# Optimization experiments

Measured on AMD Instinct MI355X. Metric: run time of the kernel, lower is better.

Reference implementation:

```python
import math
import jax, jax.numpy as jnp
import numpy as np

N, E, D, B, S, H = 16384, 196608, 256, 256, 64, 8
DH = D // H
BN_INV = 1.0 / math.sqrt(1.0 + 1e-5)  # eval-mode BN: mean=0, var=1, eps=1e-5
LOG2 = math.log(2.0)


def _mlp(x, w1, b1, w2, b2):
    # Linear -> SiLU -> Linear
    return jax.nn.silu(x @ w1 + b1) @ w2 + b2


def _bn(x, g, b):
    # BatchNorm1d in eval mode with running_mean=0, running_var=1
    return x * (BN_INV * g) + b


def _graph_ln(x, g, b):
    # pyg LayerNorm(mode='graph') called with batch=None: normalize over all nodes+features
    mu = jnp.mean(x)
    xc = x - mu
    var = jnp.mean(xc * xc)
    return xc * jax.lax.rsqrt(var + 1e-5) * g + b


def _forward(x, edge_index, edge_attr,
             node_w1, node_b1, node_w2, node_b2,
             c_w1, c_b1, c_w2, c_b2,
             bn_e_g, bn_e_b, bn_h_g, bn_h_b,
             n1l_g, n1l_b, n1a_g, n1a_b, n2_g, n2_b,
             wq, bq, wk, bk, wv, bv, wo, bo,
             aff_w1, aff_b1, aff_w2, aff_b2,
             fn_g, fn_b, fc_w1, fc_b1, fc_w2, fc_b2):
    row, col = edge_index[0], edge_index[1]

    # ---- PotNetConvGate local branch ----
    # A, B, V, U MLPs (all take node features) computed with stacked weights [4,D,D]
    hid = jax.nn.silu(jnp.einsum('nd,kdf->knf', x, node_w1) + node_b1[:, None, :])
    node_out = jnp.einsum('knf,kfg->kng', hid, node_w2) + node_b2[:, None, :]
    h_A, h_B, h_V, h_U = node_out[0], node_out[1], node_out[2], node_out[3]
    e_C = _mlp(edge_attr, c_w1, c_b1, c_w2, c_b2)  # [E,D]

    score = jax.nn.relu(_bn(h_A[row] + h_B[col] + e_C, bn_e_g, bn_e_b))  # [E,D]
    e_new = edge_attr + score

    # pyg softmax over edges grouped by destination node (col), per channel
    m = jax.ops.segment_max(e_new, col, num_segments=N)        # [N,D]
    ex = jnp.exp(e_new - m[col])
    s = jax.ops.segment_sum(ex, col, num_segments=N)           # [N,D]
    gated = ex / (s[col] + 1e-16)

    msg = gated * (h_V[col] + e_new)
    aggr = jax.ops.segment_sum(msg, col, num_segments=N)       # [N,D]
    h_local = jax.nn.silu(x + _bn(h_U + aggr, bn_h_g, bn_h_b))
    # e_out = silu(e_new + edge_attr)  # edge output, not used downstream for node output
    h_local = _bn(h_local, n1l_g, n1l_b)  # norm1_local

    # ---- global Transformer branch (equal-size graphs -> dense reshape, full mask) ----
    hd = x.reshape(B, S, D)
    q = (hd @ wq + bq).reshape(B, S, H, DH).transpose(0, 2, 1, 3)
    k = (hd @ wk + bk).reshape(B, S, H, DH).transpose(0, 2, 1, 3)
    v = (hd @ wv + bv).reshape(B, S, H, DH).transpose(0, 2, 1, 3)
    att = jax.nn.softmax(jnp.einsum('bhqd,bhkd->bhqk', q, k) / math.sqrt(DH), axis=-1)
    o = jnp.einsum('bhqk,bhkd->bhqd', att, v).transpose(0, 2, 1, 3).reshape(B, S, D)
    h_attn = (o @ wo + bo).reshape(N, D)

    h_attn = _bn(h_attn + x, n1a_g, n1a_b)  # norm1_attn
    t = jax.nn.gelu(h_attn @ aff_w1 + aff_b1, approximate=False) @ aff_w2 + aff_b2
    h_attn = _graph_ln(t + x, fn_g, fn_b)   # feed_norm

    # ---- fuse branches (mean over stacked outputs) ----
    h_new = (h_local + h_attn) * 0.5

    # ---- _ff_block: fc = Linear -> ShiftedSoftplus -> Linear ----
    ssp = jax.nn.softplus(h_new @ fc_w1 + fc_b1) - LOG2
    out = ssp @ fc_w2 + fc_b2
    return _bn(out + h_new, n2_g, n2_b)  # norm2


def setup_inputs():
    key = jax.random.key(0)
    ks = iter(jax.random.split(key, 64))
    sc = 1.0 / math.sqrt(D)
    def w(shape):
        return jax.random.normal(next(ks), shape, jnp.float32) * sc
    z = lambda *s: jnp.zeros(s, jnp.float32)
    o = lambda *s: jnp.ones(s, jnp.float32)
    return {
        'x': jax.random.normal(next(ks), (N, D), jnp.float32),
        'edge_index': jax.random.randint(next(ks), (2, E), 0, N, jnp.int32),
        'edge_attr': jax.random.normal(next(ks), (E, D), jnp.float32),
        'node_w1': w((4, D, D)), 'node_b1': z(4, D),
        'node_w2': w((4, D, D)), 'node_b2': z(4, D),
        'c_w1': w((D, D)), 'c_b1': z(D), 'c_w2': w((D, D)), 'c_b2': z(D),
        'bn_e_g': o(D), 'bn_e_b': z(D), 'bn_h_g': o(D), 'bn_h_b': z(D),
        'n1l_g': o(D), 'n1l_b': z(D), 'n1a_g': o(D), 'n1a_b': z(D),
        'n2_g': o(D), 'n2_b': z(D),
        'wq': w((D, D)), 'bq': z(D), 'wk': w((D, D)), 'bk': z(D),
        'wv': w((D, D)), 'bv': z(D), 'wo': w((D, D)), 'bo': z(D),
        'aff_w1': w((D, 2 * D)), 'aff_b1': z(2 * D),
        'aff_w2': w((2 * D, D)), 'aff_b2': z(D),
        'fn_g': o(D), 'fn_b': z(D),
        'fc_w1': w((D, 2 * D)), 'fc_b1': z(2 * D),
        'fc_w2': w((2 * D, D)), 'fc_b2': z(D),
    }


def reference(x, edge_index, edge_attr,
              node_w1, node_b1, node_w2, node_b2,
              c_w1, c_b1, c_w2, c_b2,
              bn_e_g, bn_e_b, bn_h_g, bn_h_b,
              n1l_g, n1l_b, n1a_g, n1a_b, n2_g, n2_b,
              wq, bq, wk, bk, wv, bv, wo, bo,
              aff_w1, aff_b1, aff_w2, aff_b2,
              fn_g, fn_b, fc_w1, fc_b1, fc_w2, fc_b2):
    return _forward(x, edge_index, edge_attr,
                    node_w1, node_b1, node_w2, node_b2,
                    c_w1, c_b1, c_w2, c_b2,
                    bn_e_g, bn_e_b, bn_h_g, bn_h_b,
                    n1l_g, n1l_b, n1a_g, n1a_b, n2_g, n2_b,
                    wq, bq, wk, bk, wv, bv, wo, bo,
                    aff_w1, aff_b1, aff_w2, aff_b2,
                    fn_g, fn_b, fc_w1, fc_b1, fc_w2, fc_b2)
```

## Files before the change

### kernel.cpp

```cpp
#include <hip/hip_runtime.h>
#include <hip/hip_bf16.h>
#include <stdint.h>

#define NN 16384
#define NE 196608
#define DD 256
#define ND 4194304
#define BNINV 0.9999950000374997f
#define LOG2F_ 0.6931471805599453f

typedef __attribute__((ext_vector_type(8))) short short8v;
typedef __attribute__((ext_vector_type(4))) float float4v;

__device__ __forceinline__ float b2f(__hip_bfloat16 v) { return __bfloat162float(v); }
__device__ __forceinline__ __hip_bfloat16 f2b(float v) { return __float2bfloat16(v); }

__device__ __forceinline__ void gl_lds16(const __hip_bfloat16* g, __hip_bfloat16* l) {
  __builtin_amdgcn_global_load_lds((const __attribute__((address_space(1))) void*)g,
                                   (__attribute__((address_space(3))) void*)l, 16, 0, 0);
}

__device__ __forceinline__ float rdf(const void* p, size_t i, int fl) {
  return fl ? b2f(((const __hip_bfloat16*)p)[i]) : ((const float*)p)[i];
}

#define OFF_WT    0ul
#define OFF_PB    2883584ul
#define OFF_XB    2899968ul
#define OFF_HN    11288576ul
#define OFF_HL    44843008ul
#define OFF_HIDE  61620224ul
#define OFF_EN    162283520ul
#define OFF_QKV   262946816ul
#define OFF_O     313278464ul
#define OFF_HATTN 321667072ul
#define OFF_HIDN  330055680ul
#define OFF_U     346832896ul
#define OFF_HNEW  363610112ul
#define OFF_HNEWB 380387328ul
#define OFF_TAIL  388775936ul

#define PB_NB1   0
#define PB_NB2   1024
#define PB_CB1   2048
#define PB_CB2   2304
#define PB_QKVB  2560
#define PB_BO    3328
#define PB_AB1   3584
#define PB_AB2   4096
#define PB_FB1   4352
#define PB_FB2   4864
#define PB_BNEG  5120
#define PB_BNEB  5376
#define PB_BNHG  5632
#define PB_BNHB  5888
#define PB_N1LG  6144
#define PB_N1LB  6400
#define PB_N1AG  6656
#define PB_N1AB  6912
#define PB_N2G   7168
#define PB_N2B   7424
#define PB_FNG   7680
#define PB_FNB   7936

__global__ void probe_kernel(const uint32_t* bneg_raw, int* flag) {
  if (threadIdx.x == 0 && blockIdx.x == 0)
    *flag = (bneg_raw[0] == 0x3F803F80u) ? 1 : 0;
}

struct PJobs {
  const void* src[24];
  int off[24];
  int len[24];
};

__global__ void canon_params(PJobs jb, __hip_bfloat16* PB, const int* flagp) {
  const int fl = *flagp;
  const int j = blockIdx.x;
  const void* src = jb.src[j];
  const int off = jb.off[j], len = jb.len[j];
  for (int i = threadIdx.x; i < len; i += 256) PB[off + i] = f2b(rdf(src, i, fl));
}

__global__ void canon_x(const void* x, __hip_bfloat16* XB, const int* flagp) {
  const int fl = *flagp;
  const size_t i = (size_t)blockIdx.x * 256 + threadIdx.x;
  XB[i] = f2b(rdf(x, i, fl));
}

struct TJobsF {
  const void* src[18];
  __hip_bfloat16* dst[18];
  int R[18];
  int C[18];
  int RB[18];
};

__global__ void transpose_rb(TJobsF jb, const int* flagp) {
  __shared__ __hip_bfloat16 tile[32][33];
  const int fl = *flagp;
  const int j = blockIdx.z;
  const int R = jb.R[j], C = jb.C[j], RB = jb.RB[j];
  const int c0 = blockIdx.x * 32, r0 = blockIdx.y * 32;
  if (c0 >= C || r0 >= R) return;
  const void* src = jb.src[j];
  __hip_bfloat16* dst = jb.dst[j];
  const int tx = threadIdx.x, ty = threadIdx.y;
#pragma unroll
  for (int i = 0; i < 4; ++i)
    tile[ty + i * 8][tx] = f2b(rdf(src, (size_t)(RB + r0 + ty + i * 8) * C + c0 + tx, fl));
  __syncthreads();
#pragma unroll
  for (int i = 0; i < 4; ++i)
    dst[(long)(c0 + ty + i * 8) * R + r0 + tx] = tile[tx][ty + i * 8];
}

__global__ void prep_kernel(int* counts, double* stats) {
  const int i = blockIdx.x * blockDim.x + threadIdx.x;
  if (i < NN) counts[i] = 0;
  if (i == 0) counts[NN] = 0;
  if (i < 2) stats[i] = 0.0;
}

template <int ACT, int RES, int BNM, int OUTBF, int ASRC, int DUALOUT>
__global__ __launch_bounds__(256) void gemm_bt(
    const void* __restrict__ Avp, const __hip_bfloat16* __restrict__ Wt,
    const __hip_bfloat16* __restrict__ bias, const void* __restrict__ Res,
    const __hip_bfloat16* __restrict__ bng, const __hip_bfloat16* __restrict__ bnb,
    void* __restrict__ Cout, const int* __restrict__ flagp,
    int M, int N, int K, long boff, long az, long wz, long bz, long cz) {
  __shared__ __align__(16) __hip_bfloat16 sA[128 * 32];
  __shared__ __align__(16) __hip_bfloat16 sB[128 * 32];
  const int fl = (ASRC || DUALOUT) ? *flagp : 1;
  const int z = blockIdx.z;
  const long aoff = boff + (long)z * az;
  const __hip_bfloat16* Ab = (const __hip_bfloat16*)Avp + aoff;
  const float* Af = (const float*)Avp + aoff;
  Wt += (long)z * wz;
  bias += (long)z * bz;
  const long coff = (long)z * cz;
  const int tid = threadIdx.x;
  const int lane = tid & 63;
  const int wid = tid >> 6;
  const int wm = wid >> 1, wn = wid & 1;
  const int l16 = lane & 15, lq = lane >> 4;
  const long am0 = (long)blockIdx.y * 128;
  const long bn0 = (long)blockIdx.x * 128;

  float4v acc[4][4] = {};

  const int nK = K >> 5;
  for (int kb = 0; kb < nK; ++kb) {
    if (ASRC == 1 && fl == 0) {
#pragma unroll
      for (int r = 0; r < 2; ++r) {
        const int c = tid + r * 256;
        const float* ap = Af + (am0 + (c >> 2)) * K + kb * 32 + (c & 3) * 8;
        const float4v f0 = *(const float4v*)ap;
        const float4v f1 = *(const float4v*)(ap + 4);
        short8v s;
#pragma unroll
        for (int i = 0; i < 4; ++i) {
          __hip_bfloat16 h0 = f2b(f0[i]), h1 = f2b(f1[i]);
          s[i] = *(short*)&h0;
          s[4 + i] = *(short*)&h1;
        }
        ((short8v*)sA)[c] = s;
        gl_lds16(Wt + (bn0 + (c >> 2)) * K + kb * 32 + (c & 3) * 8, sB + c * 8);
      }
    } else {
#pragma unroll
      for (int r = 0; r < 2; ++r) {
        const int c = tid + r * 256;
        gl_lds16(Ab + (am0 + (c >> 2)) * K + kb * 32 + (c & 3) * 8, sA + c * 8);
        gl_lds16(Wt + (bn0 + (c >> 2)) * K + kb * 32 + (c & 3) * 8, sB + c * 8);
      }
    }
    __syncthreads();
    const short* pA = (const short*)sA;
    const short* pB = (const short*)sB;
    short8v af[4], bv_[4];
#pragma unroll
    for (int mi = 0; mi < 4; ++mi)
      af[mi] = *(const short8v*)(pA + (wm * 64 + mi * 16 + l16) * 32 + lq * 8);
#pragma unroll
    for (int ni = 0; ni < 4; ++ni)
      bv_[ni] = *(const short8v*)(pB + (wn * 64 + ni * 16 + l16) * 32 + lq * 8);
#pragma unroll
    for (int mi = 0; mi < 4; ++mi)
#pragma unroll
      for (int ni = 0; ni < 4; ++ni)
        acc[mi][ni] =
            __builtin_amdgcn_mfma_f32_16x16x32_bf16(af[mi], bv_[ni], acc[mi][ni], 0, 0, 0);
    __syncthreads();
  }

  const __hip_bfloat16* Rb = (const __hip_bfloat16*)Res;
  const float* Rf = (const float*)Res;
#pragma unroll
  for (int mi = 0; mi < 4; ++mi) {
#pragma unroll
    for (int ni = 0; ni < 4; ++ni) {
#pragma unroll
      for (int r = 0; r < 4; ++r) {
        const long row = am0 + wm * 64 + mi * 16 + lq * 4 + r;
        const long col = bn0 + wn * 64 + ni * 16 + l16;
        float v = acc[mi][ni][r] + b2f(bias[col]);
        if (ACT == 1) v = v / (1.f + __expf(-v));
        else if (ACT == 2) v = 0.5f * v * (1.f + erff(v * 0.7071067811865476f));
        else if (ACT == 3) v = (v > 15.f ? v : log1pf(__expf(v))) - LOG2F_;
        if (RES == 1) v += b2f(Rb[row * N + col]);
        else if (RES == 2) v += Rf[row * N + col];
        if (BNM) v = v * (BNINV * b2f(bng[col])) + b2f(bnb[col]);
        if (DUALOUT) {
          if (fl) ((__hip_bfloat16*)Cout)[coff + row * N + col] = f2b(v);
          else ((float*)Cout)[coff + row * N + col] = v;
        } else if (OUTBF) {
          ((__hip_bfloat16*)Cout)[coff + row * N + col] = f2b(v);
        } else {
          ((float*)Cout)[coff + row * N + col] = v;
        }
      }
    }
  }
}

__global__ __launch_bounds__(256) void gemm_edge2(
    const __hip_bfloat16* __restrict__ A, const __hip_bfloat16* __restrict__ Wt,
    const __hip_bfloat16* __restrict__ bias, const int* __restrict__ ei,
    const void* __restrict__ eattr, const __hip_bfloat16* __restrict__ HA,
    __hip_bfloat16* __restrict__ EN, const __hip_bfloat16* __restrict__ PB,
    const int* __restrict__ perm, const int* __restrict__ flagp) {
  __shared__ __align__(16) __hip_bfloat16 sA[128 * 32];
  __shared__ __align__(16) __hip_bfloat16 sB[128 * 32];
  const int fl = *flagp;
  const int tid = threadIdx.x;
  const int lane = tid & 63;
  const int wid = tid >> 6;
  const int wm = wid >> 1, wn = wid & 1;
  const int l16 = lane & 15, lq = lane >> 4;
  const long am0 = (long)blockIdx.y * 128;
  const long bn0 = (long)blockIdx.x * 128;
  const __hip_bfloat16* HB = HA + (size_t)ND;

  float4v acc[4][4] = {};

  const int K = DD;
  for (int kb = 0; kb < (K >> 5); ++kb) {
#pragma unroll
    for (int r = 0; r < 2; ++r) {
      const int c = tid + r * 256;
      gl_lds16(A + (am0 + (c >> 2)) * K + kb * 32 + (c & 3) * 8, sA + c * 8);
      gl_lds16(Wt + (bn0 + (c >> 2)) * K + kb * 32 + (c & 3) * 8, sB + c * 8);
    }
    __syncthreads();
    const short* pA = (const short*)sA;
    const short* pB = (const short*)sB;
    short8v af[4], bv_[4];
#pragma unroll
    for (int mi = 0; mi < 4; ++mi)
      af[mi] = *(const short8v*)(pA + (wm * 64 + mi * 16 + l16) * 32 + lq * 8);
#pragma unroll
    for (int ni = 0; ni < 4; ++ni)
      bv_[ni] = *(const short8v*)(pB + (wn * 64 + ni * 16 + l16) * 32 + lq * 8);
#pragma unroll
    for (int mi = 0; mi < 4; ++mi)
#pragma unroll
      for (int ni = 0; ni < 4; ++ni)
        acc[mi][ni] =
            __builtin_amdgcn_mfma_f32_16x16x32_bf16(af[mi], bv_[ni], acc[mi][ni], 0, 0, 0);
    __syncthreads();
  }

#pragma unroll
  for (int mi = 0; mi < 4; ++mi) {
#pragma unroll
    for (int r = 0; r < 4; ++r) {
      const long row = am0 + wm * 64 + mi * 16 + lq * 4 + r;
      const long ge = row;
      const int rr = ei[ge];
      const int cc = ei[NE + ge];
      const long pe = perm[ge];
#pragma unroll
      for (int ni = 0; ni < 4; ++ni) {
        const long col = bn0 + wn * 64 + ni * 16 + l16;
        float v = acc[mi][ni][r] + b2f(bias[col]);
        v += b2f(HA[(size_t)rr * DD + col]) + b2f(HB[(size_t)cc * DD + col]);
        v = v * (BNINV * b2f(PB[PB_BNEG + col])) + b2f(PB[PB_BNEB + col]);
        v = fmaxf(v, 0.f);
        v += rdf(eattr, (size_t)ge * DD + col, fl);
        EN[(size_t)pe * DD + col] = f2b(v);
      }
    }
  }
}

__global__ void count_kernel(const int* __restrict__ ei, int* __restrict__ counts) {
  const int e = blockIdx.x * 256 + threadIdx.x;
  if (e < NE) atomicAdd(&counts[ei[NE + e]], 1);
}

__global__ __launch_bounds__(1024) void scan_kernel(int* __restrict__ counts,
                                                    int* __restrict__ cursor) {
  __shared__ int part[1024];
  const int t = threadIdx.x;
  const int base = t * 16;
  int ss = 0;
#pragma unroll
  for (int i = 0; i < 16; ++i) ss += counts[base + i];
  part[t] = ss;
  __syncthreads();
  for (int off = 1; off < 1024; off <<= 1) {
    int v = (t >= off) ? part[t - off] : 0;
    __syncthreads();
    part[t] += v;
    __syncthreads();
  }
  int run = part[t] - ss;
  for (int i = 0; i < 16; ++i) {
    const int cv = counts[base + i];
    counts[base + i] = run;
    cursor[base + i] = run;
    run += cv;
  }
  if (t == 1023) counts[NN] = run;
}

__global__ void scatter_kernel(const int* __restrict__ ei, int* __restrict__ cursor,
                               int* __restrict__ perm) {
  const int e = blockIdx.x * 256 + threadIdx.x;
  if (e < NE) {
    const int p = atomicAdd(&cursor[ei[NE + e]], 1);
    perm[e] = p;
  }
}

__global__ __launch_bounds__(256) void segment_kernel(
    const int* __restrict__ offs, const __hip_bfloat16* __restrict__ EN,
    const __hip_bfloat16* __restrict__ hV, const __hip_bfloat16* __restrict__ hU,
    const __hip_bfloat16* __restrict__ XB, const __hip_bfloat16* __restrict__ PB,
    float* __restrict__ hlocal) {
  const int n = blockIdx.x;
  const int d = threadIdx.x;
  const int beg = offs[n], end = offs[n + 1];
  float sa = 0.f, sb = 0.f;
  int p = beg;
  for (; p + 4 <= end; p += 4) {
    const float v0 = b2f(EN[(size_t)(p + 0) * DD + d]);
    const float v1 = b2f(EN[(size_t)(p + 1) * DD + d]);
    const float v2 = b2f(EN[(size_t)(p + 2) * DD + d]);
    const float v3 = b2f(EN[(size_t)(p + 3) * DD + d]);
    const float e0 = __expf(v0), e1 = __expf(v1), e2 = __expf(v2), e3 = __expf(v3);
    sa += (e0 + e1) + (e2 + e3);
    sb += (e0 * v0 + e1 * v1) + (e2 * v2 + e3 * v3);
  }
  for (; p < end; ++p) {
    const float v = b2f(EN[(size_t)p * DD + d]);
    const float e = __expf(v);
    sa += e;
    sb += e * v;
  }
  const float hv = b2f(hV[(size_t)n * DD + d]);
  const float ag = (hv * sa + sb) / (sa + 1e-16f);
  const float t1 =
      (b2f(hU[(size_t)n * DD + d]) + ag) * (BNINV * b2f(PB[PB_BNHG + d])) + b2f(PB[PB_BNHB + d]);
  float s1 = b2f(XB[(size_t)n * DD + d]) + t1;
  s1 = s1 / (1.f + __expf(-s1));
  s1 = s1 * (BNINV * b2f(PB[PB_N1LG + d])) + b2f(PB[PB_N1LB + d]);
  hlocal[(size_t)n * DD + d] = s1;
}

__global__ __launch_bounds__(256) void attn_kernel(const float* __restrict__ QKV,
                                                   __hip_bfloat16* __restrict__ O) {
  __shared__ float sq[64][33], sk[64][33], sv[64][33];
  __shared__ float sp[64][65];
  const int bh = blockIdx.x;
  const int b = bh >> 3, h = bh & 7;
  const int tid = threadIdx.x;
  const float* Q = QKV;
  const float* Kp = QKV + (size_t)ND;
  const float* Vp = QKV + 2 * (size_t)ND;
#pragma unroll
  for (int j = 0; j < 8; ++j) {
    const int idx = j * 256 + tid;
    const int s = idx >> 5, dh = idx & 31;
    const size_t ga = ((size_t)(b * 64 + s)) * DD + h * 32 + dh;
    sq[s][dh] = Q[ga];
    sk[s][dh] = Kp[ga];
    sv[s][dh] = Vp[ga];
  }
  __syncthreads();
  const int row = tid >> 2, l4 = tid & 3;
  float qr[32];
#pragma unroll
  for (int d = 0; d < 32; ++d) qr[d] = sq[row][d];
  float sc[16];
  float mx = -1e30f;
#pragma unroll
  for (int jj = 0; jj < 16; ++jj) {
    const int j = l4 * 16 + jj;
    float dot = 0.f;
#pragma unroll
    for (int d = 0; d < 32; ++d) dot += qr[d] * sk[j][d];
    dot *= 0.17677669529663687f;
    sc[jj] = dot;
    mx = fmaxf(mx, dot);
  }
  mx = fmaxf(mx, __shfl_xor(mx, 1));
  mx = fmaxf(mx, __shfl_xor(mx, 2));
  float se = 0.f;
#pragma unroll
  for (int jj = 0; jj < 16; ++jj) {
    sc[jj] = __expf(sc[jj] - mx);
    se += sc[jj];
  }
  se += __shfl_xor(se, 1);
  se += __shfl_xor(se, 2);
  const float inv = 1.f / se;
#pragma unroll
  for (int jj = 0; jj < 16; ++jj) sp[row][l4 * 16 + jj] = sc[jj] * inv;
  __syncthreads();
#pragma unroll
  for (int k8 = 0; k8 < 8; ++k8) {
    const int dh = l4 * 8 + k8;
    float acc = 0.f;
#pragma unroll
    for (int j = 0; j < 64; ++j) acc += sp[row][j] * sv[j][dh];
    O[((size_t)(b * 64 + row)) * DD + h * 32 + dh] = f2b(acc);
  }
}

__global__ __launch_bounds__(256) void stats_kernel(const float* __restrict__ U,
                                                    double* __restrict__ st) {
  double s = 0.0, s2 = 0.0;
  for (size_t i = (size_t)blockIdx.x * 256 + threadIdx.x; i < (size_t)ND;
       i += (size_t)gridDim.x * 256) {
    const double v = (double)U[i];
    s += v;
    s2 += v * v;
  }
  for (int o = 32; o > 0; o >>= 1) {
    s += __shfl_down(s, o);
    s2 += __shfl_down(s2, o);
  }
  __shared__ double wred[4][2];
  const int lane = threadIdx.x & 63, w = threadIdx.x >> 6;
  if (lane == 0) {
    wred[w][0] = s;
    wred[w][1] = s2;
  }
  __syncthreads();
  if (threadIdx.x == 0) {
    double a = 0, bb = 0;
    for (int i = 0; i < 4; ++i) {
      a += wred[i][0];
      bb += wred[i][1];
    }
    atomicAdd(&st[0], a);
    atomicAdd(&st[1], bb);
  }
}

__global__ void finalize_stats(double* st) {
  if (threadIdx.x == 0 && blockIdx.x == 0) {
    const double mu = st[0] / (double)ND;
    const double var = st[1] / (double)ND - mu * mu;
    float* f = (float*)(st + 2);
    f[0] = (float)mu;
    f[1] = (float)(1.0 / sqrt(var + 1e-5));
  }
}

__global__ void hnew_kernel(const float* __restrict__ U, const float* __restrict__ hlocal,
                            const double* __restrict__ st, const __hip_bfloat16* __restrict__ PB,
                            float* __restrict__ HNEW, __hip_bfloat16* __restrict__ HNEWB) {
  const size_t i = (size_t)blockIdx.x * 256 + threadIdx.x;
  const float* f = (const float*)(st + 2);
  const float mu = f[0], rs = f[1];
  const int d = (int)(i & 255);
  const float ha = (U[i] - mu) * rs * b2f(PB[PB_FNG + d]) + b2f(PB[PB_FNB + d]);
  const float hn = 0.5f * (hlocal[i] + ha);
  HNEW[i] = hn;
  HNEWB[i] = f2b(hn);
}

extern "C" void kernel_launch(void* const* d_in, const int* in_sizes, int n_in, void* d_out,
                              int out_size, void* d_ws, size_t ws_size, hipStream_t stream) {
  (void)in_sizes; (void)n_in; (void)out_size; (void)ws_size;
  const void* x = d_in[0];
  const int* ei = (const int*)d_in[1];
  const void* eattr = d_in[2];

  uint8_t* ws = (uint8_t*)d_ws;
  __hip_bfloat16* WT = (__hip_bfloat16*)(ws + OFF_WT);
  __hip_bfloat16* PB = (__hip_bfloat16*)(ws + OFF_PB);
  __hip_bfloat16* XB = (__hip_bfloat16*)(ws + OFF_XB);
  __hip_bfloat16* HN = (__hip_bfloat16*)(ws + OFF_HN);
  float* HL = (float*)(ws + OFF_HL);
  __hip_bfloat16* HIDE = (__hip_bfloat16*)(ws + OFF_HIDE);
  __hip_bfloat16* EN = (__hip_bfloat16*)(ws + OFF_EN);
  float* QKV = (float*)(ws + OFF_QKV);
  __hip_bfloat16* O = (__hip_bfloat16*)(ws + OFF_O);
  __hip_bfloat16* HATTN = (__hip_bfloat16*)(ws + OFF_HATTN);
  __hip_bfloat16* HIDN = (__hip_bfloat16*)(ws + OFF_HIDN);
  float* U = (float*)(ws + OFF_U);
  float* HNEW = (float*)(ws + OFF_HNEW);
  __hip_bfloat16* HNEWB = (__hip_bfloat16*)(ws + OFF_HNEWB);
  uint8_t* tail = ws + OFF_TAIL;
  int* counts = (int*)tail;
  int* cursor = (int*)(tail + 66048ul);
  int* perm = (int*)(tail + 132096ul);
  double* stats = (double*)(tail + 918528ul);
  int* flag = (int*)(tail + 918592ul);

  probe_kernel<<<1, 64, 0, stream>>>((const uint32_t*)d_in[11], flag);

  PJobs pj;
  {
    const int srcidx[24] = {4, 6, 8, 10, 22, 24, 26, 28, 30, 32, 36, 38,
                            11, 12, 13, 14, 15, 16, 17, 18, 19, 20, 33, 34};
    const int dstoff[24] = {PB_NB1, PB_NB2, PB_CB1, PB_CB2, PB_QKVB, PB_QKVB + 256,
                            PB_QKVB + 512, PB_BO, PB_AB1, PB_AB2, PB_FB1, PB_FB2,
                            PB_BNEG, PB_BNEB, PB_BNHG, PB_BNHB, PB_N1LG, PB_N1LB,
                            PB_N1AG, PB_N1AB, PB_N2G, PB_N2B, PB_FNG, PB_FNB};
    const int lens[24] = {1024, 1024, 256, 256, 256, 256, 256, 256, 512, 256, 512, 256,
                          256, 256, 256, 256, 256, 256, 256, 256, 256, 256, 256, 256};
    for (int i = 0; i < 24; ++i) {
      pj.src[i] = d_in[srcidx[i]];
      pj.off[i] = dstoff[i];
      pj.len[i] = lens[i];
    }
  }
  canon_params<<<24, 256, 0, stream>>>(pj, PB, flag);
  canon_x<<<NN, 256, 0, stream>>>(x, XB, flag);

  TJobsF jf;
  for (int j = 0; j < 4; ++j) {
    jf.src[j] = d_in[3]; jf.dst[j] = WT + j * 65536;
    jf.R[j] = 256; jf.C[j] = 256; jf.RB[j] = j * 256;
    jf.src[4 + j] = d_in[5]; jf.dst[4 + j] = WT + 262144 + j * 65536;
    jf.R[4 + j] = 256; jf.C[4 + j] = 256; jf.RB[4 + j] = j * 256;
  }
  {
    const int widx[10] = {7, 9, 21, 23, 25, 27, 29, 31, 35, 37};
    const long wdst[10] = {524288, 589824, 655360, 720896, 786432, 851968,
                           917504, 1048576, 1179648, 1310720};
    const int wR[10] = {256, 256, 256, 256, 256, 256, 256, 512, 256, 512};
    const int wC[10] = {256, 256, 256, 256, 256, 256, 512, 256, 512, 256};
    for (int j = 0; j < 10; ++j) {
      jf.src[8 + j] = d_in[widx[j]]; jf.dst[8 + j] = WT + wdst[j];
      jf.R[8 + j] = wR[j]; jf.C[8 + j] = wC[j]; jf.RB[8 + j] = 0;
    }
  }
  transpose_rb<<<dim3(16, 16, 18), dim3(32, 8), 0, stream>>>(jf, flag);

  prep_kernel<<<64, 256, 0, stream>>>(counts, stats);

  count_kernel<<<768, 256, 0, stream>>>(ei, counts);
  scan_kernel<<<1, 1024, 0, stream>>>(counts, cursor);
  scatter_kernel<<<768, 256, 0, stream>>>(ei, cursor, perm);

  gemm_bt<1, 0, 0, 1, 0, 0><<<dim3(2, 128, 4), 256, 0, stream>>>(
      XB, WT, PB + PB_NB1, nullptr, nullptr, nullptr, HIDE, flag,
      NN, DD, DD, 0, 0, 65536, 256, ND);
  gemm_bt<0, 0, 0, 1, 0, 0><<<dim3(2, 128, 4), 256, 0, stream>>>(
      HIDE, WT + 262144, PB + PB_NB2, nullptr, nullptr, nullptr, HN, flag,
      NN, DD, DD, 0, ND, 65536, 256, ND);

  gemm_bt<1, 0, 0, 1, 1, 0><<<dim3(2, 1536, 1), 256, 0, stream>>>(
      eattr, WT + 524288, PB + PB_CB1, nullptr, nullptr, nullptr, HIDE, flag,
      NE, DD, DD, 0, 0, 0, 0, 0);
  gemm_edge2<<<dim3(2, 1536, 1), 256, 0, stream>>>(
      HIDE, WT + 589824, PB + PB_CB2, ei, eattr, HN, EN, PB, perm, flag);

  segment_kernel<<<NN, 256, 0, stream>>>(counts, EN, HN + 2 * (size_t)ND,
                                         HN + 3 * (size_t)ND, XB, PB, HL);

  gemm_bt<0, 0, 0, 0, 0, 0><<<dim3(2, 128, 3), 256, 0, stream>>>(
      XB, WT + 655360, PB + PB_QKVB, nullptr, nullptr, nullptr, QKV, flag,
      NN, DD, DD, 0, 0, 65536, 256, ND);
  attn_kernel<<<2048, 256, 0, stream>>>(QKV, O);
  gemm_bt<0, 1, 1, 1, 0, 0><<<dim3(2, 128, 1), 256, 0, stream>>>(
      O, WT + 851968, PB + PB_BO, XB, PB + PB_N1AG, PB + PB_N1AB, HATTN, flag,
      NN, DD, DD, 0, 0, 0, 0, 0);

  gemm_bt<2, 0, 0, 1, 0, 0><<<dim3(4, 128, 1), 256, 0, stream>>>(
      HATTN, WT + 917504, PB + PB_AB1, nullptr, nullptr, nullptr, HIDN, flag,
      NN, 512, DD, 0, 0, 0, 0, 0);
  gemm_bt<0, 1, 0, 0, 0, 0><<<dim3(2, 128, 1), 256, 0, stream>>>(
      HIDN, WT + 1048576, PB + PB_AB2, XB, nullptr, nullptr, U, flag,
      NN, DD, 512, 0, 0, 0, 0, 0);

  stats_kernel<<<1024, 256, 0, stream>>>(U, stats);
  finalize_stats<<<1, 64, 0, stream>>>(stats);
  hnew_kernel<<<NN, 256, 0, stream>>>(U, HL, stats, PB, HNEW, HNEWB);

  gemm_bt<3, 0, 0, 1, 0, 0><<<dim3(4, 128, 1), 256, 0, stream>>>(
      HNEWB, WT + 1179648, PB + PB_FB1, nullptr, nullptr, nullptr, HIDN, flag,
      NN, 512, DD, 0, 0, 0, 0, 0);
  gemm_bt<0, 2, 1, 1, 0, 1><<<dim3(2, 128, 1), 256, 0, stream>>>(
      HIDN, WT + 1310720, PB + PB_FB2, HNEW, PB + PB_N2G, PB + PB_N2B, d_out, flag,
      NN, DD, 512, 0, 0, 0, 0, 0);
}
```

Before: 994.4 us.

## Fuse two-layer MLPs into one kernel keeping hidden activations in LDS

Replaces the separate first-layer and second-layer GEMM launches for the node MLPs and the edge MLP with a single fused kernel. Each block handles a 64-row tile across all 256 output columns, writes the SiLU hidden tile to shared memory, then runs the second GEMM from LDS. This removes the global write and re-read of the hidden activation buffer (about 100MB for edges) and two launches. In exchange, tiles are smaller with one warp per 64 columns, weights are reloaded per 64-row block, and LDS use is higher, which may lower occupancy.

```diff
diff --git a/kernel.cpp b/kernel.cpp
--- a/kernel.cpp
+++ b/kernel.cpp
@@ -29,7 +29,6 @@
 #define OFF_XB    2899968ul
 #define OFF_HN    11288576ul
 #define OFF_HL    44843008ul
-#define OFF_HIDE  61620224ul
 #define OFF_EN    162283520ul
 #define OFF_QKV   262946816ul
 #define OFF_O     313278464ul
@@ -122,7 +121,7 @@
   if (i < 2) stats[i] = 0.0;
 }
 
-template <int ACT, int RES, int BNM, int OUTBF, int ASRC, int DUALOUT>
+template <int ACT, int RES, int BNM, int OUTBF, int DUALOUT>
 __global__ __launch_bounds__(256) void gemm_bt(
     const void* __restrict__ Avp, const __hip_bfloat16* __restrict__ Wt,
     const __hip_bfloat16* __restrict__ bias, const void* __restrict__ Res,
@@ -131,11 +130,10 @@
     int M, int N, int K, long boff, long az, long wz, long bz, long cz) {
   __shared__ __align__(16) __hip_bfloat16 sA[128 * 32];
   __shared__ __align__(16) __hip_bfloat16 sB[128 * 32];
-  const int fl = (ASRC || DUALOUT) ? *flagp : 1;
+  const int fl = DUALOUT ? *flagp : 1;
   const int z = blockIdx.z;
   const long aoff = boff + (long)z * az;
   const __hip_bfloat16* Ab = (const __hip_bfloat16*)Avp + aoff;
-  const float* Af = (const float*)Avp + aoff;
   Wt += (long)z * wz;
   bias += (long)z * bz;
   const long coff = (long)z * cz;
@@ -151,30 +149,11 @@
 
   const int nK = K >> 5;
   for (int kb = 0; kb < nK; ++kb) {
-    if (ASRC == 1 && fl == 0) {
-#pragma unroll
-      for (int r = 0; r < 2; ++r) {
-        const int c = tid + r * 256;
-        const float* ap = Af + (am0 + (c >> 2)) * K + kb * 32 + (c & 3) * 8;
-        const float4v f0 = *(const float4v*)ap;
-        const float4v f1 = *(const float4v*)(ap + 4);
-        short8v s;
-#pragma unroll
-        for (int i = 0; i < 4; ++i) {
-          __hip_bfloat16 h0 = f2b(f0[i]), h1 = f2b(f1[i]);
-          s[i] = *(short*)&h0;
-          s[4 + i] = *(short*)&h1;
-        }
-        ((short8v*)sA)[c] = s;
-        gl_lds16(Wt + (bn0 + (c >> 2)) * K + kb * 32 + (c & 3) * 8, sB + c * 8);
-      }
-    } else {
-#pragma unroll
-      for (int r = 0; r < 2; ++r) {
-        const int c = tid + r * 256;
-        gl_lds16(Ab + (am0 + (c >> 2)) * K + kb * 32 + (c & 3) * 8, sA + c * 8);
-        gl_lds16(Wt + (bn0 + (c >> 2)) * K + kb * 32 + (c & 3) * 8, sB + c * 8);
-      }
+#pragma unroll
+    for (int r = 0; r < 2; ++r) {
+      const int c = tid + r * 256;
+      gl_lds16(Ab + (am0 + (c >> 2)) * K + kb * 32 + (c & 3) * 8, sA + c * 8);
+      gl_lds16(Wt + (bn0 + (c >> 2)) * K + kb * 32 + (c & 3) * 8, sB + c * 8);
     }
     __syncthreads();
     const short* pA = (const short*)sA;
@@ -225,73 +204,146 @@
   }
 }
 
-__global__ __launch_bounds__(256) void gemm_edge2(
-    const __hip_bfloat16* __restrict__ A, const __hip_bfloat16* __restrict__ Wt,
-    const __hip_bfloat16* __restrict__ bias, const int* __restrict__ ei,
-    const void* __restrict__ eattr, const __hip_bfloat16* __restrict__ HA,
-    __hip_bfloat16* __restrict__ EN, const __hip_bfloat16* __restrict__ PB,
-    const int* __restrict__ perm, const int* __restrict__ flagp) {
-  __shared__ __align__(16) __hip_bfloat16 sA[128 * 32];
-  __shared__ __align__(16) __hip_bfloat16 sB[128 * 32];
-  const int fl = *flagp;
+template <int EPI, int ASRC>
+__global__ __launch_bounds__(256) void mlp_fused(
+    const void* __restrict__ Avp, const __hip_bfloat16* __restrict__ W1t,
+    const __hip_bfloat16* __restrict__ b1, const __hip_bfloat16* __restrict__ W2t,
+    const __hip_bfloat16* __restrict__ b2, __hip_bfloat16* __restrict__ Out,
+    const int* __restrict__ ei, const void* __restrict__ eattr,
+    const __hip_bfloat16* __restrict__ HA, __hip_bfloat16* __restrict__ EN,
+    const __hip_bfloat16* __restrict__ PB, const int* __restrict__ perm,
+    const int* __restrict__ flagp, long wz, long cz) {
+  __shared__ __align__(16) __hip_bfloat16 sW[256 * 32];
+  __shared__ __align__(16) __hip_bfloat16 sH[64 * 264];
+  const int fl = (ASRC == 1) ? *flagp : 1;
+  const int z = blockIdx.z;
+  W1t += (long)z * wz;
+  W2t += (long)z * wz;
+  b1 += z * 256;
+  b2 += z * 256;
   const int tid = threadIdx.x;
   const int lane = tid & 63;
-  const int wid = tid >> 6;
-  const int wm = wid >> 1, wn = wid & 1;
+  const int wn = tid >> 6;
   const int l16 = lane & 15, lq = lane >> 4;
-  const long am0 = (long)blockIdx.y * 128;
-  const long bn0 = (long)blockIdx.x * 128;
-  const __hip_bfloat16* HB = HA + (size_t)ND;
+  const long m0 = (long)blockIdx.y * 64;
+  const __hip_bfloat16* Ab = (const __hip_bfloat16*)Avp;
+  const float* Af = (const float*)Avp;
 
   float4v acc[4][4] = {};
 
-  const int K = DD;
-  for (int kb = 0; kb < (K >> 5); ++kb) {
-#pragma unroll
-    for (int r = 0; r < 2; ++r) {
-      const int c = tid + r * 256;
-      gl_lds16(A + (am0 + (c >> 2)) * K + kb * 32 + (c & 3) * 8, sA + c * 8);
-      gl_lds16(Wt + (bn0 + (c >> 2)) * K + kb * 32 + (c & 3) * 8, sB + c * 8);
-    }
-    __syncthreads();
-    const short* pA = (const short*)sA;
-    const short* pB = (const short*)sB;
-    short8v af[4], bv_[4];
-#pragma unroll
-    for (int mi = 0; mi < 4; ++mi)
-      af[mi] = *(const short8v*)(pA + (wm * 64 + mi * 16 + l16) * 32 + lq * 8);
+  for (int kb = 0; kb < 8; ++kb) {
+    if (ASRC == 1 && fl == 0) {
+      const int arow = tid >> 2, ko = (tid & 3) * 8;
+      const float* ap = Af + (m0 + arow) * 256 + kb * 32 + ko;
+      const float4v f0 = *(const float4v*)ap;
+      const float4v f1 = *(const float4v*)(ap + 4);
+      short8v s;
+#pragma unroll
+      for (int i = 0; i < 4; ++i) {
+        __hip_bfloat16 h0 = f2b(f0[i]), h1 = f2b(f1[i]);
+        s[i] = *(short*)&h0;
+        s[4 + i] = *(short*)&h1;
+      }
+      ((short8v*)sH)[tid] = s;
+    } else {
+      gl_lds16(Ab + (m0 + (tid >> 2)) * 256 + kb * 32 + (tid & 3) * 8, sH + tid * 8);
+    }
+#pragma unroll
+    for (int r = 0; r < 4; ++r) {
+      const int c2 = r * 256 + tid;
+      gl_lds16(W1t + (c2 >> 2) * 256 + kb * 32 + (c2 & 3) * 8, sW + c2 * 8);
+    }
+    __syncthreads();
+    short8v af[4], bf_[4];
+#pragma unroll
+    for (int mi = 0; mi < 4; ++mi)
+      af[mi] = *(const short8v*)((const short*)sH + (mi * 16 + l16) * 32 + lq * 8);
 #pragma unroll
     for (int ni = 0; ni < 4; ++ni)
-      bv_[ni] = *(const short8v*)(pB + (wn * 64 + ni * 16 + l16) * 32 + lq * 8);
+      bf_[ni] = *(const short8v*)((const short*)sW + (wn * 64 + ni * 16 + l16) * 32 + lq * 8);
 #pragma unroll
     for (int mi = 0; mi < 4; ++mi)
 #pragma unroll
       for (int ni = 0; ni < 4; ++ni)
         acc[mi][ni] =
-            __builtin_amdgcn_mfma_f32_16x16x32_bf16(af[mi], bv_[ni], acc[mi][ni], 0, 0, 0);
-    __syncthreads();
-  }
-
-#pragma unroll
-  for (int mi = 0; mi < 4; ++mi) {
+            __builtin_amdgcn_mfma_f32_16x16x32_bf16(af[mi], bf_[ni], acc[mi][ni], 0, 0, 0);
+    __syncthreads();
+  }
+
+  {
+    short* hp = (short*)sH;
+#pragma unroll
+    for (int mi = 0; mi < 4; ++mi)
+#pragma unroll
+      for (int ni = 0; ni < 4; ++ni)
+#pragma unroll
+        for (int r = 0; r < 4; ++r) {
+          const int row = mi * 16 + lq * 4 + r;
+          const int col = wn * 64 + ni * 16 + l16;
+          float v = acc[mi][ni][r] + b2f(b1[col]);
+          v = v / (1.f + __expf(-v));
+          __hip_bfloat16 hb = f2b(v);
+          hp[row * 264 + col] = *(short*)&hb;
+          acc[mi][ni][r] = 0.f;
+        }
+  }
+  __syncthreads();
+
+  for (int kb = 0; kb < 8; ++kb) {
 #pragma unroll
     for (int r = 0; r < 4; ++r) {
-      const long row = am0 + wm * 64 + mi * 16 + lq * 4 + r;
-      const long ge = row;
-      const int rr = ei[ge];
-      const int cc = ei[NE + ge];
-      const long pe = perm[ge];
-#pragma unroll
-      for (int ni = 0; ni < 4; ++ni) {
-        const long col = bn0 + wn * 64 + ni * 16 + l16;
-        float v = acc[mi][ni][r] + b2f(bias[col]);
-        v += b2f(HA[(size_t)rr * DD + col]) + b2f(HB[(size_t)cc * DD + col]);
-        v = v * (BNINV * b2f(PB[PB_BNEG + col])) + b2f(PB[PB_BNEB + col]);
-        v = fmaxf(v, 0.f);
-        v += rdf(eattr, (size_t)ge * DD + col, fl);
-        EN[(size_t)pe * DD + col] = f2b(v);
+      const int c2 = r * 256 + tid;
+      gl_lds16(W2t + (c2 >> 2) * 256 + kb * 32 + (c2 & 3) * 8, sW + c2 * 8);
+    }
+    __syncthreads();
+    short8v af[4], bf_[4];
+#pragma unroll
+    for (int mi = 0; mi < 4; ++mi)
+      af[mi] = *(const short8v*)((const short*)sH + (mi * 16 + l16) * 264 + kb * 32 + lq * 8);
+#pragma unroll
+    for (int ni = 0; ni < 4; ++ni)
+      bf_[ni] = *(const short8v*)((const short*)sW + (wn * 64 + ni * 16 + l16) * 32 + lq * 8);
+#pragma unroll
+    for (int mi = 0; mi < 4; ++mi)
+#pragma unroll
+      for (int ni = 0; ni < 4; ++ni)
+        acc[mi][ni] =
+            __builtin_amdgcn_mfma_f32_16x16x32_bf16(af[mi], bf_[ni], acc[mi][ni], 0, 0, 0);
+    __syncthreads();
+  }
+
+  if (EPI == 0) {
+#pragma unroll
+    for (int mi = 0; mi < 4; ++mi)
+#pragma unroll
+      for (int ni = 0; ni < 4; ++ni)
+#pragma unroll
+        for (int r = 0; r < 4; ++r) {
+          const long row = m0 + mi * 16 + lq * 4 + r;
+          const int col = wn * 64 + ni * 16 + l16;
+          Out[(long)z * cz + row * 256 + col] = f2b(acc[mi][ni][r] + b2f(b2[col]));
+        }
+  } else {
+    const __hip_bfloat16* HB = HA + (size_t)ND;
+#pragma unroll
+    for (int mi = 0; mi < 4; ++mi)
+#pragma unroll
+      for (int r = 0; r < 4; ++r) {
+        const long ge = m0 + mi * 16 + lq * 4 + r;
+        const int rr = ei[ge];
+        const int cc = ei[NE + ge];
+        const long pe = perm[ge];
+#pragma unroll
+        for (int ni = 0; ni < 4; ++ni) {
+          const int col = wn * 64 + ni * 16 + l16;
+          float v = acc[mi][ni][r] + b2f(b2[col]);
+          v += b2f(HA[(size_t)rr * DD + col]) + b2f(HB[(size_t)cc * DD + col]);
+          v = v * (BNINV * b2f(PB[PB_BNEG + col])) + b2f(PB[PB_BNEB + col]);
+          v = fmaxf(v, 0.f);
+          v += rdf(eattr, (size_t)ge * DD + col, fl);
+          EN[(size_t)pe * DD + col] = f2b(v);
+        }
       }
-    }
   }
 }
 
@@ -497,7 +549,6 @@
   __hip_bfloat16* XB = (__hip_bfloat16*)(ws + OFF_XB);
   __hip_bfloat16* HN = (__hip_bfloat16*)(ws + OFF_HN);
   float* HL = (float*)(ws + OFF_HL);
-  __hip_bfloat16* HIDE = (__hip_bfloat16*)(ws + OFF_HIDE);
   __hip_bfloat16* EN = (__hip_bfloat16*)(ws + OFF_EN);
   float* QKV = (float*)(ws + OFF_QKV);
   __hip_bfloat16* O = (__hip_bfloat16*)(ws + OFF_O);
@@ -560,34 +611,29 @@
   scan_kernel<<<1, 1024, 0, stream>>>(counts, cursor);
   scatter_kernel<<<768, 256, 0, stream>>>(ei, cursor, perm);
 
-  gemm_bt<1, 0, 0, 1, 0, 0><<<dim3(2, 128, 4), 256, 0, stream>>>(
-      XB, WT, PB + PB_NB1, nullptr, nullptr, nullptr, HIDE, flag,
-      NN, DD, DD, 0, 0, 65536, 256, ND);
-  gemm_bt<0, 0, 0, 1, 0, 0><<<dim3(2, 128, 4), 256, 0, stream>>>(
-      HIDE, WT + 262144, PB + PB_NB2, nullptr, nullptr, nullptr, HN, flag,
-      NN, DD, DD, 0, ND, 65536, 256, ND);
-
-  gemm_bt<1, 0, 0, 1, 1, 0><<<dim3(2, 1536, 1), 256, 0, stream>>>(
-      eattr, WT + 524288, PB + PB_CB1, nullptr, nullptr, nullptr, HIDE, flag,
-      NE, DD, DD, 0, 0, 0, 0, 0);
-  gemm_edge2<<<dim3(2, 1536, 1), 256, 0, stream>>>(
-      HIDE, WT + 589824, PB + PB_CB2, ei, eattr, HN, EN, PB, perm, flag);
+  mlp_fused<0, 0><<<dim3(1, 256, 4), 256, 0, stream>>>(
+      XB, WT, PB + PB_NB1, WT + 262144, PB + PB_NB2, HN,
+      nullptr, nullptr, nullptr, nullptr, nullptr, nullptr, flag, 65536, ND);
+
+  mlp_fused<1, 1><<<dim3(1, 3072, 1), 256, 0, stream>>>(
+      eattr, WT + 524288, PB + PB_CB1, WT + 589824, PB + PB_CB2, nullptr,
+      ei, eattr, HN, EN, PB, perm, flag, 0, 0);
 
   segment_kernel<<<NN, 256, 0, stream>>>(counts, EN, HN + 2 * (size_t)ND,
                                          HN + 3 * (size_t)ND, XB, PB, HL);
 
-  gemm_bt<0, 0, 0, 0, 0, 0><<<dim3(2, 128, 3), 256, 0, stream>>>(
+  gemm_bt<0, 0, 0, 0, 0><<<dim3(2, 128, 3), 256, 0, stream>>>(
       XB, WT + 655360, PB + PB_QKVB, nullptr, nullptr, nullptr, QKV, flag,
       NN, DD, DD, 0, 0, 65536, 256, ND);
   attn_kernel<<<2048, 256, 0, stream>>>(QKV, O);
-  gemm_bt<0, 1, 1, 1, 0, 0><<<dim3(2, 128, 1), 256, 0, stream>>>(
+  gemm_bt<0, 1, 1, 1, 0><<<dim3(2, 128, 1), 256, 0, stream>>>(
       O, WT + 851968, PB + PB_BO, XB, PB + PB_N1AG, PB + PB_N1AB, HATTN, flag,
       NN, DD, DD, 0, 0, 0, 0, 0);
 
-  gemm_bt<2, 0, 0, 1, 0, 0><<<dim3(4, 128, 1), 256, 0, stream>>>(
+  gemm_bt<2, 0, 0, 1, 0><<<dim3(4, 128, 1), 256, 0, stream>>>(
       HATTN, WT + 917504, PB + PB_AB1, nullptr, nullptr, nullptr, HIDN, flag,
       NN, 512, DD, 0, 0, 0, 0, 0);
-  gemm_bt<0, 1, 0, 0, 0, 0><<<dim3(2, 128, 1), 256, 0, stream>>>(
+  gemm_bt<0, 1, 0, 0, 0><<<dim3(2, 128, 1), 256, 0, stream>>>(
       HIDN, WT + 1048576, PB + PB_AB2, XB, nullptr, nullptr, U, flag,
       NN, DD, 512, 0, 0, 0, 0, 0);
 
@@ -595,10 +641,10 @@
   finalize_stats<<<1, 64, 0, stream>>>(stats);
   hnew_kernel<<<NN, 256, 0, stream>>>(U, HL, stats, PB, HNEW, HNEWB);
 
-  gemm_bt<3, 0, 0, 1, 0, 0><<<dim3(4, 128, 1), 256, 0, stream>>>(
+  gemm_bt<3, 0, 0, 1, 0><<<dim3(4, 128, 1), 256, 0, stream>>>(
       HNEWB, WT + 1179648, PB + PB_FB1, nullptr, nullptr, nullptr, HIDN, flag,
       NN, 512, DD, 0, 0, 0, 0, 0);
-  gemm_bt<0, 2, 1, 1, 0, 1><<<dim3(2, 128, 1), 256, 0, stream>>>(
+  gemm_bt<0, 2, 1, 1, 1><<<dim3(2, 128, 1), 256, 0, stream>>>(
       HIDN, WT + 1310720, PB + PB_FB2, HNEW, PB + PB_N2G, PB + PB_N2B, d_out, flag,
       NN, DD, 512, 0, 0, 0, 0, 0);
 }
```

Result: faster. 899.2 us (-9.6%).
